# Optimization experiments

Hardware: AMD Instinct MI355X
Metric: run time of the kernel (lower is better)

## Reference

```python
import jax, jax.numpy as jnp
import numpy as np

B, S, H = 8, 2048, 768
N_SPANS = 512
MAX_SPAN_LEN = 30
WIDTH_VOCAB = 64
N_BIO, N_TYPE, N_SENS = 3, 18, 4
SPAN_DIM = H * 3 + H // 2  # 2688


def setup_inputs() -> dict:
    key = jax.random.key(0)
    ks = jax.random.split(key, 12)
    hidden = jax.random.normal(ks[0], (B, S, H), dtype=jnp.float32)
    # candidate spans: start in [0, S-MAX_SPAN_LEN), width in [1, MAX_SPAN_LEN]
    starts = jax.random.randint(ks[1], (B, N_SPANS), 0, S - MAX_SPAN_LEN)
    widths = jax.random.randint(ks[2], (B, N_SPANS), 1, MAX_SPAN_LEN + 1)
    ends = starts + widths - 1
    candidate_spans = jnp.stack([starts, ends], axis=-1).astype(jnp.int32)  # [B,N,2]
    sc = 0.02
    return {
        "hidden": hidden,
        "candidate_spans": candidate_spans,
        "width_emb": jax.random.normal(ks[3], (WIDTH_VOCAB, H // 2), dtype=jnp.float32) * sc,
        "W_prop": jax.random.normal(ks[4], (H, N_BIO), dtype=jnp.float32) * sc,
        "b_prop": jnp.zeros((N_BIO,), jnp.float32),
        "W_t1": jax.random.normal(ks[5], (SPAN_DIM, H), dtype=jnp.float32) * sc,
        "b_t1": jnp.zeros((H,), jnp.float32),
        "W_t2": jax.random.normal(ks[6], (H, N_TYPE), dtype=jnp.float32) * sc,
        "b_t2": jnp.zeros((N_TYPE,), jnp.float32),
        "W_s1": jax.random.normal(ks[7], (SPAN_DIM + N_TYPE, H), dtype=jnp.float32) * sc,
        "b_s1": jnp.zeros((H,), jnp.float32),
        "W_s2": jax.random.normal(ks[8], (H, N_SENS), dtype=jnp.float32) * sc,
        "b_s2": jnp.zeros((N_SENS,), jnp.float32),
    }


def _span_reprs(hidden, candidate_spans, width_emb):
    # hidden: [B,S,H], candidate_spans: [B,N,2] (all spans valid, 0 <= s <= e < S)
    starts = candidate_spans[..., 0]  # [B,N]
    ends = candidate_spans[..., 1]    # [B,N]
    gather = jax.vmap(lambda h, i: h[i])  # per-batch row gather
    start_h = gather(hidden, starts)  # [B,N,H]
    end_h = gather(hidden, ends)      # [B,N,H]
    # ragged mean-pool via inclusive prefix sums: sum(h[s:e+1]) = P[e+1]-P[s]
    P = jnp.concatenate(
        [jnp.zeros((hidden.shape[0], 1, hidden.shape[2]), hidden.dtype),
         jnp.cumsum(hidden, axis=1)], axis=1)  # [B,S+1,H]
    widths = ends - starts + 1  # [B,N]
    pooled = (gather(P, ends + 1) - gather(P, starts)) / widths[..., None].astype(hidden.dtype)
    width_h = width_emb[jnp.clip(widths, None, WIDTH_VOCAB - 1)]  # [B,N,H//2]
    return jnp.concatenate([start_h, end_h, pooled, width_h], axis=-1)  # [B,N,SPAN_DIM]


def reference(hidden, candidate_spans, width_emb, W_prop, b_prop,
              W_t1, b_t1, W_t2, b_t2, W_s1, b_s1, W_s2, b_s2):
    # proposal head (dropout = identity in eval)
    proposal_logits = hidden @ W_prop + b_prop  # [B,S,3]
    rep = _span_reprs(hidden, candidate_spans, width_emb)  # [B,N,2688]
    t = jax.nn.gelu(rep @ W_t1 + b_t1, approximate=False)
    type_logits = t @ W_t2 + b_t2  # [B,N,18]
    type_probs = jax.nn.softmax(type_logits, axis=-1)
    s_in = jnp.concatenate([rep, type_probs], axis=-1)  # [B,N,2706]
    s = jax.nn.gelu(s_in @ W_s1 + b_s1, approximate=False)
    sensitivity_logits = s @ W_s2 + b_s2  # [B,N,4]
    return proposal_logits, type_logits, sensitivity_logits
```

## Files before the change

### kernel.cpp

```cpp
#include <hip/hip_runtime.h>
#include <hip/hip_bf16.h>
#include <math.h>

#define Bn 8
#define Sn 2048
#define Hn 768
#define NROW 4096
#define SPAN_DIM 2688
#define NBIG 1536
#define NTYPE 18
#define NSENS 4
#define WPAD 24

#define NB_PROP 4096
#define NB_SPAN 4096
#define NB_T    2016
#define NB_SM   156
#define NB_TOTAL (NB_PROP + NB_SPAN + 2 * NB_T + NB_SM)

typedef __attribute__((ext_vector_type(8))) short short8;
typedef __attribute__((ext_vector_type(4))) float floatx4;

__device__ __forceinline__ unsigned short f2bf(float x) {
    __hip_bfloat16 h = __float2bfloat16(x);
    return *reinterpret_cast<unsigned short*>(&h);
}

__device__ __forceinline__ float bfu(unsigned short u) {
    union { float f; unsigned int i; } v;
    v.i = ((unsigned int)u) << 16;
    return v.f;
}

__device__ __forceinline__ void glds16(const void* g, void* l) {
    __builtin_amdgcn_global_load_lds(
        (const __attribute__((address_space(1))) unsigned int*)g,
        (__attribute__((address_space(3))) unsigned int*)l, 16, 0, 0);
}

__device__ __forceinline__ float gelu_exact(float v) {
    return 0.5f * v * (1.f + erff(v * 0.70710678118654752f));
}

__global__ __launch_bounds__(256) void pre_kernel(
    const float* __restrict__ hidden, const int* __restrict__ spans,
    const float* __restrict__ wemb,
    const float* __restrict__ Wp, const float* __restrict__ bp,
    const float* __restrict__ Wt1, const float* __restrict__ Ws1,
    const float* __restrict__ Wt2, const float* __restrict__ Ws2,
    float* __restrict__ out_prop, unsigned short* __restrict__ rep,
    unsigned short* __restrict__ WbigT,
    unsigned short* __restrict__ Wt2bf, unsigned short* __restrict__ Wtailbf,
    unsigned short* __restrict__ Ws2bf)
{
    __shared__ float tile[32][33];
    int id = blockIdx.x;
    int tid = threadIdx.x;

    if (id < NB_PROP) {
        int wave = tid >> 6, lane = tid & 63;
        int row = id * 4 + wave;
        const float4* h4 = (const float4*)(hidden + (size_t)row * Hn);
        float a0 = 0.f, a1 = 0.f, a2 = 0.f;
#pragma unroll
        for (int i = 0; i < 3; ++i) {
            int kc = i * 64 + lane;
            float4 h = h4[kc];
            const float* w = Wp + kc * 12;
            a0 += h.x * w[0] + h.y * w[3] + h.z * w[6] + h.w * w[9];
            a1 += h.x * w[1] + h.y * w[4] + h.z * w[7] + h.w * w[10];
            a2 += h.x * w[2] + h.y * w[5] + h.z * w[8] + h.w * w[11];
        }
#pragma unroll
        for (int off = 32; off; off >>= 1) {
            a0 += __shfl_xor(a0, off);
            a1 += __shfl_xor(a1, off);
            a2 += __shfl_xor(a2, off);
        }
        if (lane < 3) {
            float v = (lane == 0 ? a0 : (lane == 1 ? a1 : a2)) + bp[lane];
            out_prop[row * 3 + lane] = v;
        }
        return;
    }
    id -= NB_PROP;
    if (id < NB_SPAN) {
        if (tid >= 192) return;
        int n = id;
        int b = n >> 9;
        int s = spans[n * 2 + 0];
        int e = spans[n * 2 + 1];
        int w = e - s + 1;
        const float4* hb4 = (const float4*)(hidden + (size_t)b * Sn * Hn);
        unsigned short* r = rep + (size_t)n * SPAN_DIM;
        float inv_w = 1.0f / (float)w;

        float4 sv = hb4[(size_t)s * 192 + tid];
        float4 ev = hb4[(size_t)e * 192 + tid];
        float4 p0 = make_float4(0.f, 0.f, 0.f, 0.f), p1 = p0, p2 = p0, p3 = p0;
        int rr = s;
        for (; rr + 3 <= e; rr += 4) {
            float4 h0 = hb4[(size_t)(rr + 0) * 192 + tid];
            float4 h1 = hb4[(size_t)(rr + 1) * 192 + tid];
            float4 h2 = hb4[(size_t)(rr + 2) * 192 + tid];
            float4 h3 = hb4[(size_t)(rr + 3) * 192 + tid];
            p0.x += h0.x; p0.y += h0.y; p0.z += h0.z; p0.w += h0.w;
            p1.x += h1.x; p1.y += h1.y; p1.z += h1.z; p1.w += h1.w;
            p2.x += h2.x; p2.y += h2.y; p2.z += h2.z; p2.w += h2.w;
            p3.x += h3.x; p3.y += h3.y; p3.z += h3.z; p3.w += h3.w;
        }
        for (; rr <= e; ++rr) {
            float4 h = hb4[(size_t)rr * 192 + tid];
            p0.x += h.x; p0.y += h.y; p0.z += h.z; p0.w += h.w;
        }
        float4 pv;
        pv.x = ((p0.x + p1.x) + (p2.x + p3.x)) * inv_w;
        pv.y = ((p0.y + p1.y) + (p2.y + p3.y)) * inv_w;
        pv.z = ((p0.z + p1.z) + (p2.z + p3.z)) * inv_w;
        pv.w = ((p0.w + p1.w) + (p2.w + p3.w)) * inv_w;

        *(ushort4*)&r[tid * 4] =
            make_ushort4(f2bf(sv.x), f2bf(sv.y), f2bf(sv.z), f2bf(sv.w));
        *(ushort4*)&r[Hn + tid * 4] =
            make_ushort4(f2bf(ev.x), f2bf(ev.y), f2bf(ev.z), f2bf(ev.w));
        *(ushort4*)&r[2 * Hn + tid * 4] =
            make_ushort4(f2bf(pv.x), f2bf(pv.y), f2bf(pv.z), f2bf(pv.w));
        if (tid < 96) {
            int wi = w > 63 ? 63 : w;
            float4 wv = ((const float4*)wemb)[wi * 96 + tid];
            *(ushort4*)&r[3 * Hn + tid * 4] =
                make_ushort4(f2bf(wv.x), f2bf(wv.y), f2bf(wv.z), f2bf(wv.w));
        }
        return;
    }
    id -= NB_SPAN;
    if (id < 2 * NB_T) {
        int z = id / NB_T, l = id - z * NB_T;
        const float* W = (z == 0) ? Wt1 : Ws1;
        unsigned short* Wt = WbigT + (size_t)z * Hn * SPAN_DIM;
        int k0 = (l % 84) * 32, n0 = (l / 84) * 32;
        int tx = tid & 31, ty = tid >> 5;
#pragma unroll
        for (int i = 0; i < 32; i += 8)
            tile[ty + i][tx] = W[(size_t)(k0 + ty + i) * Hn + n0 + tx];
        __syncthreads();
#pragma unroll
        for (int i = 0; i < 32; i += 8)
            Wt[(size_t)(n0 + ty + i) * SPAN_DIM + k0 + tx] = f2bf(tile[tx][ty + i]);
        return;
    }
    id -= 2 * NB_T;
    {
        int idx = id * 256 + tid;
        const int N1 = Hn * WPAD;
        const int N2 = 2 * N1;
        const int N3 = N2 + Hn * NSENS;
        if (idx < N1) {
            int k = idx / WPAD, o = idx - k * WPAD;
            Wt2bf[idx] = (o < NTYPE) ? f2bf(Wt2[k * NTYPE + o]) : 0;
        } else if (idx < N2) {
            int j = idx - N1;
            int k = j / WPAD, o = j - k * WPAD;
            Wtailbf[j] = (o < NTYPE) ? f2bf(Ws1[(size_t)(SPAN_DIM + o) * Hn + k]) : 0;
        } else if (idx < N3) {
            int j = idx - N2;
            Ws2bf[j] = f2bf(Ws2[j]);
        }
    }
}

__global__ __launch_bounds__(256, 3) void gemm_fused(
    const unsigned short* __restrict__ A,
    const unsigned short* __restrict__ Bt,
    const float* __restrict__ bt1, const float* __restrict__ bs1,
    float* __restrict__ obuf)
{
    const int BK = 64;
    __shared__ unsigned short As[2][128 * BK];
    __shared__ unsigned short Bs[2][64 * BK];

    int tid = threadIdx.x, wave = tid >> 6, lane = tid & 63;
    int bid = blockIdx.x;
    int xcd = bid & 7, g = bid >> 3;
    int bx = xcd * 4 + (g / 24);
    int by = g % 24;
    int m0 = bx * 128, n0 = by * 64;

    int wr = (wave >> 1) * 64;
    int wc = (wave & 1) * 32;
    int fr = lane & 15;
    int fc = lane >> 4;

    const unsigned short* gA[4];
#pragma unroll
    for (int j = 0; j < 4; ++j) {
        int d = tid + j * 256;
        int r = d >> 3, c = (d & 7) ^ (r & 7);
        gA[j] = A + (size_t)(m0 + r) * SPAN_DIM + c * 8;
    }
    const unsigned short* gB[2];
#pragma unroll
    for (int j = 0; j < 2; ++j) {
        int d = tid + j * 256;
        int r = d >> 3, c = (d & 7) ^ (r & 7);
        gB[j] = Bt + (size_t)(n0 + r) * SPAN_DIM + c * 8;
    }
    int offA[4], offB[2];
#pragma unroll
    for (int j = 0; j < 4; ++j) offA[j] = j * 2048 + wave * 512;
#pragma unroll
    for (int j = 0; j < 2; ++j) offB[j] = j * 2048 + wave * 512;

    floatx4 acc[4][2] = {};

    glds16(gA[0], &As[0][offA[0]]);
    glds16(gA[1], &As[0][offA[1]]);
    glds16(gA[2], &As[0][offA[2]]);
    glds16(gA[3], &As[0][offA[3]]);
    glds16(gB[0], &Bs[0][offB[0]]);
    glds16(gB[1], &Bs[0][offB[1]]);

    const int NITER = SPAN_DIM / BK;
    for (int i = 0; i < NITER; ++i) {
        int cur = i & 1;
        __syncthreads();
        if (i + 1 < NITER) {
            int k1 = (i + 1) * BK;
            int nxt = cur ^ 1;
            glds16(gA[0] + k1, &As[nxt][offA[0]]);
            glds16(gA[1] + k1, &As[nxt][offA[1]]);
            glds16(gA[2] + k1, &As[nxt][offA[2]]);
            glds16(gA[3] + k1, &As[nxt][offA[3]]);
            glds16(gB[0] + k1, &Bs[nxt][offB[0]]);
            glds16(gB[1] + k1, &Bs[nxt][offB[1]]);
        }
#pragma unroll
        for (int half = 0; half < 2; ++half) {
            int cb = half * 4 + fc;
            short8 af[4], bf[2];
#pragma unroll
            for (int ii = 0; ii < 4; ++ii) {
                int r = wr + ii * 16 + fr;
                af[ii] = *(const short8*)&As[cur][((r << 3) | (cb ^ (r & 7))) * 8];
            }
#pragma unroll
            for (int ii = 0; ii < 2; ++ii) {
                int r = wc + ii * 16 + fr;
                bf[ii] = *(const short8*)&Bs[cur][((r << 3) | (cb ^ (r & 7))) * 8];
            }
#pragma unroll
            for (int mi = 0; mi < 4; ++mi)
#pragma unroll
                for (int ni = 0; ni < 2; ++ni)
                    acc[mi][ni] = __builtin_amdgcn_mfma_f32_16x16x32_bf16(
                        af[mi], bf[ni], acc[mi][ni], 0, 0, 0);
        }
    }

    bool isT = (n0 < Hn);
    const float* bias = isT ? bt1 : (bs1 - Hn);
    int cr = (lane >> 4) * 4;
#pragma unroll
    for (int mi = 0; mi < 4; ++mi) {
#pragma unroll
        for (int ni = 0; ni < 2; ++ni) {
            int col = n0 + wc + ni * 16 + fr;
            float bv = bias[col];
#pragma unroll
            for (int r = 0; r < 4; ++r) {
                int row = m0 + wr + mi * 16 + cr + r;
                float v = acc[mi][ni][r] + bv;
                if (isT) v = gelu_exact(v);
                obuf[(size_t)row * NBIG + col] = v;
            }
        }
    }
}

__global__ __launch_bounds__(256) void heads_kernel(
    const float* __restrict__ obuf, const unsigned short* __restrict__ Wt2bf,
    const float* __restrict__ bt2, const unsigned short* __restrict__ Wtailbf,
    const unsigned short* __restrict__ Ws2bf, const float* __restrict__ bs2,
    float* __restrict__ out_type, float* __restrict__ out_sens)
{
    int wave = threadIdx.x >> 6, lane = threadIdx.x & 63;
    int row = blockIdx.x * 4 + wave;
    const float* tr = obuf + (size_t)row * NBIG;

    float t[12];
    {
        const float4* t4 = (const float4*)(tr + lane * 12);
        float4 a = t4[0], b = t4[1], c = t4[2];
        t[0] = a.x; t[1] = a.y; t[2]  = a.z; t[3]  = a.w;
        t[4] = b.x; t[5] = b.y; t[6]  = b.z; t[7]  = b.w;
        t[8] = c.x; t[9] = c.y; t[10] = c.z; t[11] = c.w;
    }
    float acc[NTYPE] = {};
    const unsigned short* wp = Wt2bf + (size_t)lane * 12 * WPAD;
#pragma unroll
    for (int j = 0; j < 12; ++j) {
        short8 w0 = *(const short8*)(wp + j * WPAD);
        short8 w1 = *(const short8*)(wp + j * WPAD + 8);
        ushort4 w2 = *(const ushort4*)(wp + j * WPAD + 16);
        float tv = t[j];
#pragma unroll
        for (int o = 0; o < 8; ++o) acc[o] += tv * bfu((unsigned short)w0[o]);
#pragma unroll
        for (int o = 0; o < 8; ++o) acc[8 + o] += tv * bfu((unsigned short)w1[o]);
        acc[16] += tv * bfu(w2.x);
        acc[17] += tv * bfu(w2.y);
    }
#pragma unroll
    for (int o = 0; o < NTYPE; ++o)
#pragma unroll
        for (int off = 32; off; off >>= 1) acc[o] += __shfl_xor(acc[o], off);

    float mx = -1e30f;
#pragma unroll
    for (int o = 0; o < NTYPE; ++o) { acc[o] += bt2[o]; mx = fmaxf(mx, acc[o]); }
    {
        float lv = 0.f;
#pragma unroll
        for (int o = 0; o < NTYPE; ++o) lv = (lane == o) ? acc[o] : lv;
        if (lane < NTYPE) out_type[row * NTYPE + lane] = lv;
    }
    float pr[NTYPE], sum = 0.f;
#pragma unroll
    for (int o = 0; o < NTYPE; ++o) { pr[o] = expf(acc[o] - mx); sum += pr[o]; }
    float inv = 1.f / sum;
#pragma unroll
    for (int o = 0; o < NTYPE; ++o) pr[o] *= inv;

    float s[12];
    {
        const float4* s4 = (const float4*)(tr + Hn + lane * 12);
        float4 a = s4[0], b = s4[1], c = s4[2];
        s[0] = a.x; s[1] = a.y; s[2]  = a.z; s[3]  = a.w;
        s[4] = b.x; s[5] = b.y; s[6]  = b.z; s[7]  = b.w;
        s[8] = c.x; s[9] = c.y; s[10] = c.z; s[11] = c.w;
    }
    float acc2[NSENS] = {};
    const unsigned short* wt = Wtailbf + (size_t)lane * 12 * WPAD;
    const unsigned short* w2p = Ws2bf + (size_t)lane * 12 * NSENS;
#pragma unroll
    for (int j = 0; j < 12; ++j) {
        short8 a0 = *(const short8*)(wt + j * WPAD);
        short8 a1 = *(const short8*)(wt + j * WPAD + 8);
        ushort4 a2 = *(const ushort4*)(wt + j * WPAD + 16);
        float tl = 0.f;
#pragma unroll
        for (int o = 0; o < 8; ++o) tl += pr[o] * bfu((unsigned short)a0[o]);
#pragma unroll
        for (int o = 0; o < 8; ++o) tl += pr[8 + o] * bfu((unsigned short)a1[o]);
        tl += pr[16] * bfu(a2.x) + pr[17] * bfu(a2.y);
        float v = gelu_exact(s[j] + tl);
        ushort4 wv = *(const ushort4*)(w2p + j * NSENS);
        acc2[0] += v * bfu(wv.x);
        acc2[1] += v * bfu(wv.y);
        acc2[2] += v * bfu(wv.z);
        acc2[3] += v * bfu(wv.w);
    }
#pragma unroll
    for (int o = 0; o < NSENS; ++o)
#pragma unroll
        for (int off = 32; off; off >>= 1) acc2[o] += __shfl_xor(acc2[o], off);
    {
        float lv = 0.f;
#pragma unroll
        for (int o = 0; o < NSENS; ++o) lv = (lane == o) ? (acc2[o] + bs2[o]) : lv;
        if (lane < NSENS) out_sens[row * NSENS + lane] = lv;
    }
}

extern "C" void kernel_launch(void* const* d_in, const int* in_sizes, int n_in,
                              void* d_out, int out_size, void* d_ws, size_t ws_size,
                              hipStream_t stream)
{
    const float* hidden = (const float*)d_in[0];
    const int*   spans  = (const int*)d_in[1];
    const float* wemb   = (const float*)d_in[2];
    const float* Wp     = (const float*)d_in[3];
    const float* bp     = (const float*)d_in[4];
    const float* Wt1    = (const float*)d_in[5];
    const float* bt1    = (const float*)d_in[6];
    const float* Wt2    = (const float*)d_in[7];
    const float* bt2    = (const float*)d_in[8];
    const float* Ws1    = (const float*)d_in[9];
    const float* bs1    = (const float*)d_in[10];
    const float* Ws2    = (const float*)d_in[11];
    const float* bs2    = (const float*)d_in[12];

    float* out      = (float*)d_out;
    float* out_prop = out;
    float* out_type = out + Bn * Sn * 3;
    float* out_sens = out_type + NROW * NTYPE;

    unsigned short* rep = (unsigned short*)d_ws;
    float* obuf = (float*)(rep + (size_t)NROW * SPAN_DIM);
    unsigned short* WbigT = (unsigned short*)(obuf + (size_t)NROW * NBIG);
    unsigned short* Wt2bf   = WbigT + (size_t)NBIG * SPAN_DIM;
    unsigned short* Wtailbf = Wt2bf + Hn * WPAD;
    unsigned short* Ws2bf   = Wtailbf + Hn * WPAD;

    pre_kernel<<<NB_TOTAL, 256, 0, stream>>>(
        hidden, spans, wemb, Wp, bp, Wt1, Ws1, Wt2, Ws2,
        out_prop, rep, WbigT, Wt2bf, Wtailbf, Ws2bf);

    gemm_fused<<<768, 256, 0, stream>>>(rep, WbigT, bt1, bs1, obuf);

    heads_kernel<<<NROW / 4, 256, 0, stream>>>(
        obuf, Wt2bf, bt2, Wtailbf, Ws2bf, bs2, out_type, out_sens);
}
```

Baseline: 230.0 us.

## Use 128x128 GEMM tiles without double buffering and store bf16 intermediates

The GEMM tile grows from 128x64 to 128x128 per block, with a 4x4 MFMA accumulator per wave. The LDS double buffering is removed in favour of a single buffer with two barriers per K step, and the XCD-aware block remapping is replaced by a plain 2D grid. The intermediate activation buffer is stored as bf16 instead of fp32, which halves write and read traffic, and the heads kernel is rewritten to read it with coalesced ushort4 loads. The risks are exposed global-load latency now that prefetch is gone, fewer blocks (384 instead of 768) on the device, and a small accuracy loss from bf16 rounding of the intermediates.

Result: faster. 222.5 us (-3.3%).

```diff
diff --git a/kernel.cpp b/kernel.cpp
--- a/kernel.cpp
+++ b/kernel.cpp
@@ -169,92 +169,72 @@
     }
 }
 
-__global__ __launch_bounds__(256, 3) void gemm_fused(
+__global__ __launch_bounds__(256, 2) void gemm_fused(
     const unsigned short* __restrict__ A,
     const unsigned short* __restrict__ Bt,
     const float* __restrict__ bt1, const float* __restrict__ bs1,
-    float* __restrict__ obuf)
+    unsigned short* __restrict__ obuf)
 {
     const int BK = 64;
-    __shared__ unsigned short As[2][128 * BK];
-    __shared__ unsigned short Bs[2][64 * BK];
+    __shared__ unsigned short As[128 * BK];
+    __shared__ unsigned short Bs[128 * BK];
 
     int tid = threadIdx.x, wave = tid >> 6, lane = tid & 63;
-    int bid = blockIdx.x;
-    int xcd = bid & 7, g = bid >> 3;
-    int bx = xcd * 4 + (g / 24);
-    int by = g % 24;
-    int m0 = bx * 128, n0 = by * 64;
+    int m0 = blockIdx.x * 128, n0 = blockIdx.y * 128;
 
     int wr = (wave >> 1) * 64;
-    int wc = (wave & 1) * 32;
+    int wc = (wave & 1) * 64;
     int fr = lane & 15;
     int fc = lane >> 4;
 
     const unsigned short* gA[4];
+    const unsigned short* gB[4];
 #pragma unroll
     for (int j = 0; j < 4; ++j) {
         int d = tid + j * 256;
         int r = d >> 3, c = (d & 7) ^ (r & 7);
         gA[j] = A + (size_t)(m0 + r) * SPAN_DIM + c * 8;
-    }
-    const unsigned short* gB[2];
-#pragma unroll
-    for (int j = 0; j < 2; ++j) {
-        int d = tid + j * 256;
-        int r = d >> 3, c = (d & 7) ^ (r & 7);
         gB[j] = Bt + (size_t)(n0 + r) * SPAN_DIM + c * 8;
     }
-    int offA[4], offB[2];
-#pragma unroll
-    for (int j = 0; j < 4; ++j) offA[j] = j * 2048 + wave * 512;
-#pragma unroll
-    for (int j = 0; j < 2; ++j) offB[j] = j * 2048 + wave * 512;
-
-    floatx4 acc[4][2] = {};
-
-    glds16(gA[0], &As[0][offA[0]]);
-    glds16(gA[1], &As[0][offA[1]]);
-    glds16(gA[2], &As[0][offA[2]]);
-    glds16(gA[3], &As[0][offA[3]]);
-    glds16(gB[0], &Bs[0][offB[0]]);
-    glds16(gB[1], &Bs[0][offB[1]]);
-
-    const int NITER = SPAN_DIM / BK;
-    for (int i = 0; i < NITER; ++i) {
-        int cur = i & 1;
+    int off[4];
+#pragma unroll
+    for (int j = 0; j < 4; ++j) off[j] = j * 2048 + wave * 512;
+
+    floatx4 acc[4][4] = {};
+
+    for (int k0 = 0; k0 < SPAN_DIM; k0 += BK) {
+        glds16(gA[0] + k0, &As[off[0]]);
+        glds16(gA[1] + k0, &As[off[1]]);
+        glds16(gA[2] + k0, &As[off[2]]);
+        glds16(gA[3] + k0, &As[off[3]]);
+        glds16(gB[0] + k0, &Bs[off[0]]);
+        glds16(gB[1] + k0, &Bs[off[1]]);
+        glds16(gB[2] + k0, &Bs[off[2]]);
+        glds16(gB[3] + k0, &Bs[off[3]]);
         __syncthreads();
-        if (i + 1 < NITER) {
-            int k1 = (i + 1) * BK;
-            int nxt = cur ^ 1;
-            glds16(gA[0] + k1, &As[nxt][offA[0]]);
-            glds16(gA[1] + k1, &As[nxt][offA[1]]);
-            glds16(gA[2] + k1, &As[nxt][offA[2]]);
-            glds16(gA[3] + k1, &As[nxt][offA[3]]);
-            glds16(gB[0] + k1, &Bs[nxt][offB[0]]);
-            glds16(gB[1] + k1, &Bs[nxt][offB[1]]);
-        }
+
 #pragma unroll
         for (int half = 0; half < 2; ++half) {
             int cb = half * 4 + fc;
-            short8 af[4], bf[2];
-#pragma unroll
-            for (int ii = 0; ii < 4; ++ii) {
-                int r = wr + ii * 16 + fr;
-                af[ii] = *(const short8*)&As[cur][((r << 3) | (cb ^ (r & 7))) * 8];
+            short8 af[4], bf[4];
+#pragma unroll
+            for (int i = 0; i < 4; ++i) {
+                int r = wr + i * 16 + fr;
+                af[i] = *(const short8*)&As[((r << 3) | (cb ^ (r & 7))) * 8];
             }
 #pragma unroll
-            for (int ii = 0; ii < 2; ++ii) {
-                int r = wc + ii * 16 + fr;
-                bf[ii] = *(const short8*)&Bs[cur][((r << 3) | (cb ^ (r & 7))) * 8];
+            for (int i = 0; i < 4; ++i) {
+                int r = wc + i * 16 + fr;
+                bf[i] = *(const short8*)&Bs[((r << 3) | (cb ^ (r & 7))) * 8];
             }
 #pragma unroll
             for (int mi = 0; mi < 4; ++mi)
 #pragma unroll
-                for (int ni = 0; ni < 2; ++ni)
+                for (int ni = 0; ni < 4; ++ni)
                     acc[mi][ni] = __builtin_amdgcn_mfma_f32_16x16x32_bf16(
                         af[mi], bf[ni], acc[mi][ni], 0, 0, 0);
         }
+        __syncthreads();
     }
 
     bool isT = (n0 < Hn);
@@ -263,7 +243,7 @@
 #pragma unroll
     for (int mi = 0; mi < 4; ++mi) {
 #pragma unroll
-        for (int ni = 0; ni < 2; ++ni) {
+        for (int ni = 0; ni < 4; ++ni) {
             int col = n0 + wc + ni * 16 + fr;
             float bv = bias[col];
 #pragma unroll
@@ -271,44 +251,41 @@
                 int row = m0 + wr + mi * 16 + cr + r;
                 float v = acc[mi][ni][r] + bv;
                 if (isT) v = gelu_exact(v);
-                obuf[(size_t)row * NBIG + col] = v;
+                obuf[(size_t)row * NBIG + col] = f2bf(v);
             }
         }
     }
 }
 
 __global__ __launch_bounds__(256) void heads_kernel(
-    const float* __restrict__ obuf, const unsigned short* __restrict__ Wt2bf,
+    const unsigned short* __restrict__ obuf, const unsigned short* __restrict__ Wt2bf,
     const float* __restrict__ bt2, const unsigned short* __restrict__ Wtailbf,
     const unsigned short* __restrict__ Ws2bf, const float* __restrict__ bs2,
     float* __restrict__ out_type, float* __restrict__ out_sens)
 {
     int wave = threadIdx.x >> 6, lane = threadIdx.x & 63;
     int row = blockIdx.x * 4 + wave;
-    const float* tr = obuf + (size_t)row * NBIG;
-
-    float t[12];
-    {
-        const float4* t4 = (const float4*)(tr + lane * 12);
-        float4 a = t4[0], b = t4[1], c = t4[2];
-        t[0] = a.x; t[1] = a.y; t[2]  = a.z; t[3]  = a.w;
-        t[4] = b.x; t[5] = b.y; t[6]  = b.z; t[7]  = b.w;
-        t[8] = c.x; t[9] = c.y; t[10] = c.z; t[11] = c.w;
-    }
+    const ushort4* tr4 = (const ushort4*)(obuf + (size_t)row * NBIG);
+
     float acc[NTYPE] = {};
-    const unsigned short* wp = Wt2bf + (size_t)lane * 12 * WPAD;
-#pragma unroll
-    for (int j = 0; j < 12; ++j) {
-        short8 w0 = *(const short8*)(wp + j * WPAD);
-        short8 w1 = *(const short8*)(wp + j * WPAD + 8);
-        ushort4 w2 = *(const ushort4*)(wp + j * WPAD + 16);
-        float tv = t[j];
-#pragma unroll
-        for (int o = 0; o < 8; ++o) acc[o] += tv * bfu((unsigned short)w0[o]);
-#pragma unroll
-        for (int o = 0; o < 8; ++o) acc[8 + o] += tv * bfu((unsigned short)w1[o]);
-        acc[16] += tv * bfu(w2.x);
-        acc[17] += tv * bfu(w2.y);
+#pragma unroll
+    for (int i = 0; i < 3; ++i) {
+        ushort4 tc = tr4[lane + i * 64];
+        float tv[4] = {bfu(tc.x), bfu(tc.y), bfu(tc.z), bfu(tc.w)};
+#pragma unroll
+        for (int j = 0; j < 4; ++j) {
+            int k = (lane + i * 64) * 4 + j;
+            const unsigned short* wp = Wt2bf + (size_t)k * WPAD;
+            short8 w0 = *(const short8*)wp;
+            short8 w1 = *(const short8*)(wp + 8);
+            ushort4 w2 = *(const ushort4*)(wp + 16);
+#pragma unroll
+            for (int o = 0; o < 8; ++o) acc[o] += tv[j] * bfu((unsigned short)w0[o]);
+#pragma unroll
+            for (int o = 0; o < 8; ++o) acc[8 + o] += tv[j] * bfu((unsigned short)w1[o]);
+            acc[16] += tv[j] * bfu(w2.x);
+            acc[17] += tv[j] * bfu(w2.y);
+        }
     }
 #pragma unroll
     for (int o = 0; o < NTYPE; ++o)
@@ -331,34 +308,32 @@
 #pragma unroll
     for (int o = 0; o < NTYPE; ++o) pr[o] *= inv;
 
-    float s[12];
-    {
-        const float4* s4 = (const float4*)(tr + Hn + lane * 12);
-        float4 a = s4[0], b = s4[1], c = s4[2];
-        s[0] = a.x; s[1] = a.y; s[2]  = a.z; s[3]  = a.w;
-        s[4] = b.x; s[5] = b.y; s[6]  = b.z; s[7]  = b.w;
-        s[8] = c.x; s[9] = c.y; s[10] = c.z; s[11] = c.w;
-    }
+    const ushort4* sp4 = (const ushort4*)(obuf + (size_t)row * NBIG + Hn);
     float acc2[NSENS] = {};
-    const unsigned short* wt = Wtailbf + (size_t)lane * 12 * WPAD;
-    const unsigned short* w2p = Ws2bf + (size_t)lane * 12 * NSENS;
-#pragma unroll
-    for (int j = 0; j < 12; ++j) {
-        short8 a0 = *(const short8*)(wt + j * WPAD);
-        short8 a1 = *(const short8*)(wt + j * WPAD + 8);
-        ushort4 a2 = *(const ushort4*)(wt + j * WPAD + 16);
-        float tl = 0.f;
-#pragma unroll
-        for (int o = 0; o < 8; ++o) tl += pr[o] * bfu((unsigned short)a0[o]);
-#pragma unroll
-        for (int o = 0; o < 8; ++o) tl += pr[8 + o] * bfu((unsigned short)a1[o]);
-        tl += pr[16] * bfu(a2.x) + pr[17] * bfu(a2.y);
-        float v = gelu_exact(s[j] + tl);
-        ushort4 wv = *(const ushort4*)(w2p + j * NSENS);
-        acc2[0] += v * bfu(wv.x);
-        acc2[1] += v * bfu(wv.y);
-        acc2[2] += v * bfu(wv.z);
-        acc2[3] += v * bfu(wv.w);
+#pragma unroll
+    for (int i = 0; i < 3; ++i) {
+        ushort4 sc = sp4[lane + i * 64];
+        float sv[4] = {bfu(sc.x), bfu(sc.y), bfu(sc.z), bfu(sc.w)};
+#pragma unroll
+        for (int j = 0; j < 4; ++j) {
+            int k = (lane + i * 64) * 4 + j;
+            const unsigned short* wt = Wtailbf + (size_t)k * WPAD;
+            short8 a0 = *(const short8*)wt;
+            short8 a1 = *(const short8*)(wt + 8);
+            ushort4 a2 = *(const ushort4*)(wt + 16);
+            float tl = 0.f;
+#pragma unroll
+            for (int o = 0; o < 8; ++o) tl += pr[o] * bfu((unsigned short)a0[o]);
+#pragma unroll
+            for (int o = 0; o < 8; ++o) tl += pr[8 + o] * bfu((unsigned short)a1[o]);
+            tl += pr[16] * bfu(a2.x) + pr[17] * bfu(a2.y);
+            float v = gelu_exact(sv[j] + tl);
+            ushort4 wv = *(const ushort4*)(Ws2bf + (size_t)k * NSENS);
+            acc2[0] += v * bfu(wv.x);
+            acc2[1] += v * bfu(wv.y);
+            acc2[2] += v * bfu(wv.z);
+            acc2[3] += v * bfu(wv.w);
+        }
     }
 #pragma unroll
     for (int o = 0; o < NSENS; ++o)
@@ -395,9 +370,9 @@
     float* out_type = out + Bn * Sn * 3;
     float* out_sens = out_type + NROW * NTYPE;
 
-    unsigned short* rep = (unsigned short*)d_ws;
-    float* obuf = (float*)(rep + (size_t)NROW * SPAN_DIM);
-    unsigned short* WbigT = (unsigned short*)(obuf + (size_t)NROW * NBIG);
+    unsigned short* rep  = (unsigned short*)d_ws;
+    unsigned short* obuf = rep + (size_t)NROW * SPAN_DIM;
+    unsigned short* WbigT = obuf + (size_t)NROW * NBIG;
     unsigned short* Wt2bf   = WbigT + (size_t)NBIG * SPAN_DIM;
     unsigned short* Wtailbf = Wt2bf + Hn * WPAD;
     unsigned short* Ws2bf   = Wtailbf + Hn * WPAD;
@@ -406,7 +381,8 @@
         hidden, spans, wemb, Wp, bp, Wt1, Ws1, Wt2, Ws2,
         out_prop, rep, WbigT, Wt2bf, Wtailbf, Ws2bf);
 
-    gemm_fused<<<768, 256, 0, stream>>>(rep, WbigT, bt1, bs1, obuf);
+    dim3 gg(NROW / 128, NBIG / 128);
+    gemm_fused<<<gg, 256, 0, stream>>>(rep, WbigT, bt1, bs1, obuf);
 
     heads_kernel<<<NROW / 4, 256, 0, stream>>>(
         obuf, Wt2bf, bt2, Wtailbf, Ws2bf, bs2, out_type, out_sens);
```
